# Performance work log

Hardware: AMD Instinct MI355X
Metric: run time of the kernel (lower is better)

Reference implementation:

```python
import jax, jax.numpy as jnp
import numpy as np

SCALES = (0, 1, 2, 3)
SIGMA_NSQ = 2.0
SIGMA_MAX_INV = 4.0 / (255.0 * 255.0)
GAIN_LIMIT = 100.0  # NEG=False
EPS = 1e-10


def gaussian_kernel_2d(N):
    sigma = N / 5.0
    x = jnp.arange(N, dtype=jnp.float32) - (N - 1) / 2.0
    g = jnp.exp(-(x * x) / (2.0 * sigma * sigma))
    k = jnp.outer(g, g)
    return (k / jnp.sum(k))[None, None]  # [1,1,N,N]


def reflect_pad(x, p):
    return jnp.pad(x, ((0, 0), (0, 0), (p, p), (p, p)), mode='reflect')


def conv2d(x, w, stride=1, groups=1):
    return jax.lax.conv_general_dilated(
        x, w, (stride, stride), 'VALID',
        dimension_numbers=('NCHW', 'OIHW', 'NCHW'),
        feature_group_count=groups)


def vif_num_den(ref, dist):
    ref = ref - 128.0
    dist = dist - 128.0
    h, w = ref.shape[-2], ref.shape[-1]
    nums, dens = [], []
    for scale in SCALES:
        N = 2 ** (4 - scale) + 1
        win = gaussian_kernel_2d(N)
        p = (N - 1) // 2
        if scale > 0:
            h, w = h // 2, w // 2
            ref = conv2d(reflect_pad(ref, p), win, stride=2)[:, :, :h, :w]
            dist = conv2d(reflect_pad(dist, p), win, stride=2)[:, :, :h, :w]
        win5 = jnp.tile(win, (5, 1, 1, 1))  # grouped conv, 5 channels
        inp = jnp.concatenate([ref, dist, ref * ref, dist * dist, ref * dist], axis=1)
        out = conv2d(reflect_pad(inp, p), win5, groups=5)  # [b,5,h,w]
        mu1, mu2, s1, s2, s12 = [out[:, i:i + 1] for i in range(5)]
        s1 = jax.nn.relu(s1 - mu1 * mu1)
        s2 = jax.nn.relu(s2 - mu2 * mu2)
        s12 = s12 - mu1 * mu2
        g = s12 / (s1 + EPS)
        sv = s2 - g * s12
        m1 = s1 < EPS
        g = jnp.where(m1, 0.0, g)
        sv = jnp.where(m1, s2, sv)
        s1 = jnp.where(m1, 0.0, s1)
        m2 = s2 < EPS
        g = jnp.where(m2, 0.0, g)
        sv = jnp.where(m2, 0.0, sv)
        sv = jnp.where(g < 0.0, s2, sv)
        g = jax.nn.relu(g)
        sv = jnp.where(sv <= EPS, EPS, sv)
        g = jnp.minimum(g, GAIN_LIMIT)
        num_ar = jnp.log2(1.0 + g * g * s1 / (sv + SIGMA_NSQ))
        den_ar = jnp.log2(1.0 + s1 / SIGMA_NSQ)
        num_ar = jnp.where(s12 < 0.0, 0.0, num_ar)
        m3 = s1 < SIGMA_NSQ
        num_ar = jnp.where(m3, 1.0 - s2 * SIGMA_MAX_INV, num_ar)
        den_ar = jnp.where(m3, 1.0, den_ar)
        nums.append(jnp.sum(num_ar, axis=(-1, -2, -3)))
        dens.append(jnp.sum(den_ar, axis=(-1, -2, -3)))
    return jnp.stack(nums, axis=-1), jnp.stack(dens, axis=-1)


def setup_inputs() -> dict:
    key = jax.random.key(0)
    k1, k2 = jax.random.split(key)
    shape = (4, 1, 1080, 1920)
    ref = jax.random.uniform(k1, shape, dtype=jnp.float32) * 255.0
    dist = jax.random.uniform(k2, shape, dtype=jnp.float32) * 255.0
    return {"ref": ref, "dist": dist}


def reference(ref, dist):
    num, den = vif_num_den(ref, dist)
    return num / den  # VIF features per scale, shape [b, 4]
```

## Files before the change

kernel.cpp:

```cpp
#include <hip/hip_runtime.h>
#include <math.h>

#define VIF_EPS       1e-10f
#define SIGMA_NSQ     2.0f
#define SIGMA_MAX_INV (4.0f / (255.0f * 255.0f))
#define GAIN_LIMIT    100.0f

typedef float v2f __attribute__((ext_vector_type(2)));
typedef float v4f __attribute__((ext_vector_type(4)));

static __device__ __forceinline__ v2f splat2(float s) {
    v2f v; v.x = s; v.y = s; return v;
}

__device__ __forceinline__ int reflect_idx(int i, int n) {
    i = (i < 0) ? -i : i;
    i = (i >= n) ? (2 * n - 2 - i) : i;
    return i;
}

template <int N>
__device__ __forceinline__ void fill_weights_global(float* gw) {
    const float sigma = (float)N / 5.0f;
    const float denom = 2.0f * sigma * sigma;
    float tmp[N];
    float s = 0.0f;
    for (int i = 0; i < N; ++i) {
        float x = (float)i - (float)(N - 1) * 0.5f;
        float g = expf(-(x * x) / denom);
        tmp[i] = g;
        s += g;
    }
    for (int i = 0; i < N; ++i) gw[i] = tmp[i] / s;
}

__global__ __launch_bounds__(64) void init_weights_kernel(float* __restrict__ gw) {
    const int tid = threadIdx.x;
    if (tid == 0) fill_weights_global<17>(gw + 0);
    else if (tid == 1) fill_weights_global<9>(gw + 17);
    else if (tid == 2) fill_weights_global<5>(gw + 26);
    else if (tid == 3) fill_weights_global<3>(gw + 31);
}

__host__ __device__ constexpr int w_off(int N) {
    return (N == 17) ? 0 : (N == 9) ? 17 : (N == 5) ? 26 : 31;
}

constexpr int tile_w(int N) { return (256 - (N - 1)) & ~3; }

template <int N>
struct alignas(16) StatsSmem {
    v2f   a[8][256];
    v2f   bq[8][256];
    float c[8][256];
};
template <int N>
struct alignas(16) DownSmem {
    v2f vb[8][252];
};

template <int N>
__device__ __forceinline__ void stats_body(
    StatsSmem<N>& sm, const float* __restrict__ refp, const float* __restrict__ distp,
    const float* __restrict__ gw,
    int h, int w, float shift, double2* __restrict__ partial,
    int sy, int sx, int bx, int b) {
    constexpr int P   = (N - 1) / 2;
    constexpr int TW  = tile_w(N);
    constexpr int TH  = 8;
    constexpr int LR  = TH + 2 * P;
    constexpr int XG4 = TW / 4;
    constexpr int NT  = TH * XG4;
    constexpr int REPS = (NT + 255) / 256;

    const int tid = threadIdx.x;
    const int ytile = bx % sy;
    const int xtile = bx / sy;
    const int x0 = xtile * TW;
    const int y0 = ytile * TH;

    float wr[N];
#pragma unroll
    for (int j = 0; j < N; ++j) wr[j] = gw[j];

    {
        const int cc = tid;
        const int gx = reflect_idx(x0 + cc - P, w);
        const float* rbase = refp  + (size_t)b * h * w;
        const float* dbase = distp + (size_t)b * h * w;

        float rrow[LR], drow[LR];
        const int rowlo = y0 - P;
        if (rowlo >= 0 && rowlo + LR <= h) {
            unsigned voff = (unsigned)(rowlo * w + gx) * 4u;
            const unsigned vstep = (unsigned)w * 4u;
#pragma unroll
            for (int i = 0; i < LR; ++i) {
                rrow[i] = *(const float*)((const char*)rbase + voff);
                drow[i] = *(const float*)((const char*)dbase + voff);
                voff += vstep;
            }
        } else {
#pragma unroll
            for (int i = 0; i < LR; ++i) {
                const int gy = reflect_idx(rowlo + i, h);
                const size_t o = (size_t)gy * w + gx;
                rrow[i] = rbase[o];
                drow[i] = dbase[o];
            }
        }

        v2f accA[TH], accB[TH];
        float accC[TH];
#pragma unroll
        for (int t = 0; t < TH; ++t) {
            accA[t] = splat2(0.f);
            accB[t] = splat2(0.f);
            accC[t] = 0.f;
        }
#pragma unroll
        for (int i = 0; i < LR; ++i) {
            const float r = rrow[i] - shift;
            const float d = drow[i] - shift;
            v2f rd; rd.x = r; rd.y = d;
            v2f sq = rd * rd;
            const float x = r * d;
#pragma unroll
            for (int t = 0; t < TH; ++t) {
                const int j = i - t;
                if (j >= 0 && j < N) {
                    const float wj = wr[j];
                    accA[t] += splat2(wj) * rd;
                    accB[t] += splat2(wj) * sq;
                    accC[t] += wj * x;
                }
            }
        }
#pragma unroll
        for (int t = 0; t < TH; ++t) {
            sm.a[t][cc]  = accA[t];
            sm.bq[t][cc] = accB[t];
            sm.c[t][cc]  = accC[t];
        }
    }
    __syncthreads();

    float num_v = 0.f, den_v = 0.f;
    {
        constexpr int WC  = N + 3;
        constexpr int F4C = (WC + 3) / 4;
#pragma unroll
        for (int rep = 0; rep < REPS; ++rep) {
            const int task = tid + 256 * rep;
            if (task < NT) {
                const int row = task / XG4;
                const int xg  = task - row * XG4;

                v2f muA[4], muB[4];
                float muC[4];
#pragma unroll
                for (int q = 0; q < 4; ++q) {
                    muA[q] = splat2(0.f);
                    muB[q] = splat2(0.f);
                    muC[q] = 0.f;
                }

                const v4f* A4 = (const v4f*)&sm.a[row][xg * 4];
                const v4f* B4 = (const v4f*)&sm.bq[row][xg * 4];
#pragma unroll
                for (int f = 0; f < WC / 2; ++f) {
                    v4f ta = A4[f];
                    v4f tb = B4[f];
#pragma unroll
                    for (int hlf = 0; hlf < 2; ++hlf) {
                        const int k = 2 * f + hlf;
                        v2f pa = hlf ? __builtin_shufflevector(ta, ta, 2, 3)
                                     : __builtin_shufflevector(ta, ta, 0, 1);
                        v2f pb = hlf ? __builtin_shufflevector(tb, tb, 2, 3)
                                     : __builtin_shufflevector(tb, tb, 0, 1);
#pragma unroll
                        for (int q = 0; q < 4; ++q) {
                            const int j = k - q;
                            if (j >= 0 && j < N) {
                                const float wj = wr[j];
                                muA[q] += splat2(wj) * pa;
                                muB[q] += splat2(wj) * pb;
                            }
                        }
                    }
                }
                {
                    const v4f* C4 = (const v4f*)&sm.c[row][xg * 4];
#pragma unroll
                    for (int f = 0; f < F4C; ++f) {
                        v4f t = C4[f];
#pragma unroll
                        for (int e = 0; e < 4; ++e) {
                            const int k = 4 * f + e;
                            const float x = (e == 0) ? t.x : (e == 1) ? t.y
                                          : (e == 2) ? t.z : t.w;
#pragma unroll
                            for (int q = 0; q < 4; ++q) {
                                const int j = k - q;
                                if (j >= 0 && j < N) muC[q] += wr[j] * x;
                            }
                        }
                    }
                }

                const int gy = y0 + row;
#pragma unroll
                for (int q = 0; q < 4; ++q) {
                    int gx = x0 + xg * 4 + q;
                    if (gx < w && gy < h) {
                        float mu1 = muA[q].x, mu2 = muA[q].y;
                        float s1  = fmaxf(0.f, muB[q].x - mu1 * mu1);
                        float s2  = fmaxf(0.f, muB[q].y - mu2 * mu2);
                        float s12 = muC[q] - mu1 * mu2;

                        float g  = s12 / (s1 + VIF_EPS);
                        float sv = s2 - g * s12;
                        if (s1 < VIF_EPS) { g = 0.f; sv = s2; s1 = 0.f; }
                        if (s2 < VIF_EPS) { g = 0.f; sv = 0.f; }
                        if (g  < 0.f)     { sv = s2; g = 0.f; }
                        if (sv <= VIF_EPS) sv = VIF_EPS;
                        g = fminf(g, GAIN_LIMIT);

                        float num_ar = __log2f(1.f + g * g * s1 / (sv + SIGMA_NSQ));
                        float den_ar = __log2f(1.f + s1 / SIGMA_NSQ);
                        if (s12 < 0.f) num_ar = 0.f;
                        if (s1 < SIGMA_NSQ) { num_ar = 1.f - s2 * SIGMA_MAX_INV; den_ar = 1.f; }
                        num_v += num_ar;
                        den_v += den_ar;
                    }
                }
            }
        }
    }

#pragma unroll
    for (int off = 32; off > 0; off >>= 1) {
        num_v += __shfl_down(num_v, off);
        den_v += __shfl_down(den_v, off);
    }
    __syncthreads();
    float* rs = reinterpret_cast<float*>(&sm);
    const int wid = tid >> 6, lane = tid & 63;
    if (lane == 0) { rs[wid] = num_v; rs[4 + wid] = den_v; }
    __syncthreads();
    if (tid == 0) {
        float ns = rs[0] + rs[1] + rs[2] + rs[3];
        float ds = rs[4] + rs[5] + rs[6] + rs[7];
        partial[(size_t)b * (sy * sx) + bx] = make_double2((double)ns, (double)ds);
    }
}

template <int N>
__device__ __forceinline__ void down_body(
    DownSmem<N>& sm, const float* __restrict__ rin, const float* __restrict__ din,
    const float* __restrict__ gw,
    float* __restrict__ rout, float* __restrict__ dout,
    int h, int w, int h2, int w2, float shift, int dgx, int bx, int b) {
    constexpr int P   = (N - 1) / 2;
    constexpr int TOW = 120, TOH = 8;
    constexpr int IC  = 2 * (TOW - 1) + N;
    constexpr int NR  = 2 * (TOH - 1) + N;
    constexpr int XG4 = TOW / 4;
    constexpr int WL  = N + 6;

    float wr[N];
#pragma unroll
    for (int j = 0; j < N; ++j) wr[j] = gw[j];

    const int tid = threadIdx.x;
    const int xt  = bx % dgx;
    const int yt  = bx / dgx;
    const int x0  = xt * TOW;
    const int y0  = yt * TOH;

    if (tid < IC) {
        const int gx = reflect_idx(2 * x0 - P + tid, w);
        const int rowlo = 2 * y0 - P;
        const float* rbase = rin + (size_t)b * h * w;
        const float* dbase = din + (size_t)b * h * w;

        float rr[NR], dd[NR];
        const bool interior = (rowlo >= 0) && (rowlo + NR <= h);
        if (interior) {
            unsigned voff = (unsigned)(rowlo * w + gx) * 4u;
            const unsigned vstep = (unsigned)w * 4u;
#pragma unroll
            for (int i = 0; i < NR; ++i) {
                rr[i] = *(const float*)((const char*)rbase + voff);
                dd[i] = *(const float*)((const char*)dbase + voff);
                voff += vstep;
            }
        } else {
#pragma unroll
            for (int i = 0; i < NR; ++i) {
                const int gy = reflect_idx(rowlo + i, h);
                const size_t o = (size_t)gy * w + gx;
                rr[i] = rbase[o];
                dd[i] = dbase[o];
            }
        }

        v2f acc[TOH];
#pragma unroll
        for (int t = 0; t < TOH; ++t) acc[t] = splat2(0.f);
#pragma unroll
        for (int i = 0; i < NR; ++i) {
            v2f x; x.x = rr[i] - shift; x.y = dd[i] - shift;
#pragma unroll
            for (int t = 0; t < TOH; ++t) {
                const int j = i - 2 * t;
                if (j >= 0 && j < N) acc[t] += splat2(wr[j]) * x;
            }
        }
#pragma unroll
        for (int t = 0; t < TOH; ++t) sm.vb[t][tid] = acc[t];
    }
    __syncthreads();

    if (tid < TOH * XG4) {
        const int row = tid / XG4;
        const int xg  = tid - row * XG4;

        v2f o[4];
#pragma unroll
        for (int q = 0; q < 4; ++q) o[q] = splat2(0.f);

        const v4f* s4 = (const v4f*)&sm.vb[row][8 * xg];
#pragma unroll
        for (int f = 0; f < (WL + 1) / 2; ++f) {
            v4f t = s4[f];
#pragma unroll
            for (int hlf = 0; hlf < 2; ++hlf) {
                const int k = 2 * f + hlf;
                v2f p = hlf ? __builtin_shufflevector(t, t, 2, 3)
                            : __builtin_shufflevector(t, t, 0, 1);
#pragma unroll
                for (int q = 0; q < 4; ++q) {
                    const int j = k - 2 * q;
                    if (j >= 0 && j < N) o[q] += splat2(wr[j]) * p;
                }
            }
        }
        const int gy = y0 + row;
        if (gy < h2) {
            float* rp = rout + (size_t)b * h2 * w2 + (size_t)gy * w2 + x0 + 4 * xg;
            float* dp = dout + (size_t)b * h2 * w2 + (size_t)gy * w2 + x0 + 4 * xg;
            *(float4*)rp = make_float4(o[0].x, o[1].x, o[2].x, o[3].x);
            *(float4*)dp = make_float4(o[0].y, o[1].y, o[2].y, o[3].y);
        }
    }
}

template <int NS, int ND>
__global__ __launch_bounds__(256) void fused_kernel(
    const float* __restrict__ sref, const float* __restrict__ sdist,
    const float* __restrict__ gw,
    int sh, int sw, float sshift, double2* __restrict__ partial, int sy, int sx,
    float* __restrict__ drout, float* __restrict__ ddout,
    int dh2, int dw2, int dgx, int nStats) {
    __shared__ union {
        StatsSmem<NS> s;
        DownSmem<ND>  d;
    } u;
    const int bx = blockIdx.x;
    const int b  = blockIdx.z;
    if (bx < nStats)
        stats_body<NS>(u.s, sref, sdist, gw + w_off(NS), sh, sw, sshift,
                       partial, sy, sx, bx, b);
    else
        down_body<ND>(u.d, sref, sdist, gw + w_off(ND), drout, ddout,
                      sh, sw, dh2, dw2, sshift, dgx, bx - nStats, b);
}

template <int N>
__global__ __launch_bounds__(256) void stats_only_kernel(
    const float* __restrict__ refp, const float* __restrict__ distp,
    const float* __restrict__ gw,
    int h, int w, float shift, double2* __restrict__ partial, int sy, int sx) {
    __shared__ StatsSmem<N> sm;
    stats_body<N>(sm, refp, distp, gw + w_off(N), h, w, shift, partial,
                  sy, sx, blockIdx.x, blockIdx.z);
}

__global__ __launch_bounds__(256) void reduce_kernel(
    const double2* __restrict__ part, float* __restrict__ out,
    int4 bases, int4 counts) {
    __shared__ double sn[4], sd[4];
    const int s = blockIdx.x & 3;
    const int b = blockIdx.x >> 2;
    const int base = (&bases.x)[s];
    const int cnt  = (&counts.x)[s];
    const double2* p = part + base + (size_t)b * cnt;

    double ns = 0.0, ds = 0.0;
    for (int i = threadIdx.x; i < cnt; i += 256) {
        double2 v = p[i];
        ns += v.x;
        ds += v.y;
    }
#pragma unroll
    for (int off = 32; off > 0; off >>= 1) {
        ns += __shfl_down(ns, off);
        ds += __shfl_down(ds, off);
    }
    const int wid = threadIdx.x >> 6, lane = threadIdx.x & 63;
    if (lane == 0) { sn[wid] = ns; sd[wid] = ds; }
    __syncthreads();
    if (threadIdx.x == 0) {
        double Nv = sn[0] + sn[1] + sn[2] + sn[3];
        double Dv = sd[0] + sd[1] + sd[2] + sd[3];
        out[b * 4 + s] = (float)(Nv / Dv);
    }
}

extern "C" void kernel_launch(void* const* d_in, const int* in_sizes, int n_in,
                              void* d_out, int out_size, void* d_ws, size_t ws_size,
                              hipStream_t stream) {
    const float* ref  = (const float*)d_in[0];
    const float* dist = (const float*)d_in[1];
    float* out = (float*)d_out;

    const int B = 4;
    const int H0 = 1080, W0 = 1920;
    const int H1 = 540,  W1 = 960;
    const int H2 = 270,  W2 = 480;
    const int H3 = 135,  W3 = 240;

    char*  ws  = (char*)d_ws;
    size_t off = 0;
    auto alloc = [&](size_t bytes) -> void* {
        void* p = ws + off;
        off += (bytes + 255) & ~(size_t)255;
        return p;
    };
    float* gw    = (float*)alloc(34 * sizeof(float));
    float* ref1  = (float*)alloc((size_t)B * H1 * W1 * 4);
    float* dist1 = (float*)alloc((size_t)B * H1 * W1 * 4);
    float* ref2  = (float*)alloc((size_t)B * H2 * W2 * 4);
    float* dist2 = (float*)alloc((size_t)B * H2 * W2 * 4);
    float* ref3  = (float*)alloc((size_t)B * H3 * W3 * 4);
    float* dist3 = (float*)alloc((size_t)B * H3 * W3 * 4);

    const int sx0 = (W0 + tile_w(17) - 1) / tile_w(17), sy0 = (H0 + 7) / 8;
    const int sx1 = (W1 + tile_w(9)  - 1) / tile_w(9),  sy1 = (H1 + 7) / 8;
    const int sx2 = (W2 + tile_w(5)  - 1) / tile_w(5),  sy2 = (H2 + 7) / 8;
    const int sx3 = (W3 + tile_w(3)  - 1) / tile_w(3),  sy3 = (H3 + 7) / 8;
    const int n0 = sx0 * sy0, n1 = sx1 * sy1, n2 = sx2 * sy2, n3 = sx3 * sy3;

    const int dgx1 = W1 / 120, nD1 = dgx1 * ((H1 + 7) / 8);
    const int dgx2 = W2 / 120, nD2 = dgx2 * ((H2 + 7) / 8);
    const int dgx3 = W3 / 120, nD3 = dgx3 * ((H3 + 7) / 8);

    double2* part = (double2*)alloc((size_t)B * (n0 + n1 + n2 + n3) * sizeof(double2));
    double2* p0 = part;
    double2* p1 = p0 + (size_t)B * n0;
    double2* p2 = p1 + (size_t)B * n1;
    double2* p3 = p2 + (size_t)B * n2;

    dim3 blk(256);

    init_weights_kernel<<<1, 64, 0, stream>>>(gw);

    fused_kernel<17, 9><<<dim3(n0 + nD1, 1, B), blk, 0, stream>>>(
        ref, dist, gw, H0, W0, 128.0f, p0, sy0, sx0,
        ref1, dist1, H1, W1, dgx1, n0);

    fused_kernel<9, 5><<<dim3(n1 + nD2, 1, B), blk, 0, stream>>>(
        ref1, dist1, gw, H1, W1, 0.0f, p1, sy1, sx1,
        ref2, dist2, H2, W2, dgx2, n1);

    fused_kernel<5, 3><<<dim3(n2 + nD3, 1, B), blk, 0, stream>>>(
        ref2, dist2, gw, H2, W2, 0.0f, p2, sy2, sx2,
        ref3, dist3, H3, W3, dgx3, n2);

    stats_only_kernel<3><<<dim3(n3, 1, B), blk, 0, stream>>>(
        ref3, dist3, gw, H3, W3, 0.0f, p3, sy3, sx3);

    reduce_kernel<<<16, 256, 0, stream>>>(
        part, out,
        make_int4(0, B * n0, B * (n0 + n1), B * (n0 + n1 + n2)),
        make_int4(n0, n1, n2, n3));
}
```

Before: 171.3 us.

## Shrink stats shared-memory staging to five rows with a two-phase reuse

The stats kernel now stores only five rows of vertical-pass results in shared memory instead of eight. It first computes the horizontal pass for rows 0-4, then overwrites slots 0-2 with rows 5-7 (row 4 stays in slot 4) and handles the remaining tasks. The smaller shared-memory footprint is meant to let more blocks fit per CU. In exchange it adds an extra barrier, and keeps the row 5-7 accumulators live in registers across the first phase, which may raise register pressure.

```diff
diff --git a/kernel.cpp b/kernel.cpp
--- a/kernel.cpp
+++ b/kernel.cpp
@@ -50,9 +50,9 @@
 
 template <int N>
 struct alignas(16) StatsSmem {
-    v2f   a[8][256];
-    v2f   bq[8][256];
-    float c[8][256];
+    v2f   a[5][256];
+    v2f   bq[5][256];
+    float c[5][256];
 };
 template <int N>
 struct alignas(16) DownSmem {
@@ -71,7 +71,7 @@
     constexpr int LR  = TH + 2 * P;
     constexpr int XG4 = TW / 4;
     constexpr int NT  = TH * XG4;
-    constexpr int REPS = (NT + 255) / 256;
+    static_assert(5 * XG4 >= 256, "phase 2a tasks must fit rows 0..4");
 
     const int tid = threadIdx.x;
     const int ytile = bx % sy;
@@ -83,6 +83,8 @@
 #pragma unroll
     for (int j = 0; j < N; ++j) wr[j] = gw[j];
 
+    v2f accA[TH], accB[TH];
+    float accC[TH];
     {
         const int cc = tid;
         const int gx = reflect_idx(x0 + cc - P, w);
@@ -110,8 +112,6 @@
             }
         }
 
-        v2f accA[TH], accB[TH];
-        float accC[TH];
 #pragma unroll
         for (int t = 0; t < TH; ++t) {
             accA[t] = splat2(0.f);
@@ -137,104 +137,121 @@
             }
         }
 #pragma unroll
-        for (int t = 0; t < TH; ++t) {
-            sm.a[t][cc]  = accA[t];
-            sm.bq[t][cc] = accB[t];
-            sm.c[t][cc]  = accC[t];
+        for (int t = 0; t < 5; ++t) {
+            sm.a[t][tid]  = accA[t];
+            sm.bq[t][tid] = accB[t];
+            sm.c[t][tid]  = accC[t];
         }
     }
     __syncthreads();
 
     float num_v = 0.f, den_v = 0.f;
-    {
-        constexpr int WC  = N + 3;
-        constexpr int F4C = (WC + 3) / 4;
-#pragma unroll
-        for (int rep = 0; rep < REPS; ++rep) {
-            const int task = tid + 256 * rep;
-            if (task < NT) {
-                const int row = task / XG4;
-                const int xg  = task - row * XG4;
-
-                v2f muA[4], muB[4];
-                float muC[4];
+    constexpr int WC  = N + 3;
+    constexpr int F4C = (WC + 3) / 4;
+
+    auto do_task = [&](int task, int slot) {
+        const int row = task / XG4;
+        const int xg  = task - row * XG4;
+
+        v2f muA[4], muB[4];
+        float muC[4];
+#pragma unroll
+        for (int q = 0; q < 4; ++q) {
+            muA[q] = splat2(0.f);
+            muB[q] = splat2(0.f);
+            muC[q] = 0.f;
+        }
+
+        const v4f* A4 = (const v4f*)&sm.a[slot][xg * 4];
+        const v4f* B4 = (const v4f*)&sm.bq[slot][xg * 4];
+#pragma unroll
+        for (int f = 0; f < WC / 2; ++f) {
+            v4f ta = A4[f];
+            v4f tb = B4[f];
+#pragma unroll
+            for (int hlf = 0; hlf < 2; ++hlf) {
+                const int k = 2 * f + hlf;
+                v2f pa = hlf ? __builtin_shufflevector(ta, ta, 2, 3)
+                             : __builtin_shufflevector(ta, ta, 0, 1);
+                v2f pb = hlf ? __builtin_shufflevector(tb, tb, 2, 3)
+                             : __builtin_shufflevector(tb, tb, 0, 1);
 #pragma unroll
                 for (int q = 0; q < 4; ++q) {
-                    muA[q] = splat2(0.f);
-                    muB[q] = splat2(0.f);
-                    muC[q] = 0.f;
-                }
-
-                const v4f* A4 = (const v4f*)&sm.a[row][xg * 4];
-                const v4f* B4 = (const v4f*)&sm.bq[row][xg * 4];
-#pragma unroll
-                for (int f = 0; f < WC / 2; ++f) {
-                    v4f ta = A4[f];
-                    v4f tb = B4[f];
-#pragma unroll
-                    for (int hlf = 0; hlf < 2; ++hlf) {
-                        const int k = 2 * f + hlf;
-                        v2f pa = hlf ? __builtin_shufflevector(ta, ta, 2, 3)
-                                     : __builtin_shufflevector(ta, ta, 0, 1);
-                        v2f pb = hlf ? __builtin_shufflevector(tb, tb, 2, 3)
-                                     : __builtin_shufflevector(tb, tb, 0, 1);
-#pragma unroll
-                        for (int q = 0; q < 4; ++q) {
-                            const int j = k - q;
-                            if (j >= 0 && j < N) {
-                                const float wj = wr[j];
-                                muA[q] += splat2(wj) * pa;
-                                muB[q] += splat2(wj) * pb;
-                            }
-                        }
+                    const int j = k - q;
+                    if (j >= 0 && j < N) {
+                        const float wj = wr[j];
+                        muA[q] += splat2(wj) * pa;
+                        muB[q] += splat2(wj) * pb;
                     }
                 }
-                {
-                    const v4f* C4 = (const v4f*)&sm.c[row][xg * 4];
-#pragma unroll
-                    for (int f = 0; f < F4C; ++f) {
-                        v4f t = C4[f];
-#pragma unroll
-                        for (int e = 0; e < 4; ++e) {
-                            const int k = 4 * f + e;
-                            const float x = (e == 0) ? t.x : (e == 1) ? t.y
-                                          : (e == 2) ? t.z : t.w;
-#pragma unroll
-                            for (int q = 0; q < 4; ++q) {
-                                const int j = k - q;
-                                if (j >= 0 && j < N) muC[q] += wr[j] * x;
-                            }
-                        }
+            }
+        }
+        {
+            const v4f* C4 = (const v4f*)&sm.c[slot][xg * 4];
+#pragma unroll
+            for (int f = 0; f < F4C; ++f) {
+                v4f t = C4[f];
+#pragma unroll
+                for (int e = 0; e < 4; ++e) {
+                    const int k = 4 * f + e;
+                    const float x = (e == 0) ? t.x : (e == 1) ? t.y
+                                  : (e == 2) ? t.z : t.w;
+#pragma unroll
+                    for (int q = 0; q < 4; ++q) {
+                        const int j = k - q;
+                        if (j >= 0 && j < N) muC[q] += wr[j] * x;
                     }
                 }
-
-                const int gy = y0 + row;
-#pragma unroll
-                for (int q = 0; q < 4; ++q) {
-                    int gx = x0 + xg * 4 + q;
-                    if (gx < w && gy < h) {
-                        float mu1 = muA[q].x, mu2 = muA[q].y;
-                        float s1  = fmaxf(0.f, muB[q].x - mu1 * mu1);
-                        float s2  = fmaxf(0.f, muB[q].y - mu2 * mu2);
-                        float s12 = muC[q] - mu1 * mu2;
-
-                        float g  = s12 / (s1 + VIF_EPS);
-                        float sv = s2 - g * s12;
-                        if (s1 < VIF_EPS) { g = 0.f; sv = s2; s1 = 0.f; }
-                        if (s2 < VIF_EPS) { g = 0.f; sv = 0.f; }
-                        if (g  < 0.f)     { sv = s2; g = 0.f; }
-                        if (sv <= VIF_EPS) sv = VIF_EPS;
-                        g = fminf(g, GAIN_LIMIT);
-
-                        float num_ar = __log2f(1.f + g * g * s1 / (sv + SIGMA_NSQ));
-                        float den_ar = __log2f(1.f + s1 / SIGMA_NSQ);
-                        if (s12 < 0.f) num_ar = 0.f;
-                        if (s1 < SIGMA_NSQ) { num_ar = 1.f - s2 * SIGMA_MAX_INV; den_ar = 1.f; }
-                        num_v += num_ar;
-                        den_v += den_ar;
-                    }
-                }
-            }
+            }
+        }
+
+        const int gy = y0 + row;
+#pragma unroll
+        for (int q = 0; q < 4; ++q) {
+            int gx = x0 + xg * 4 + q;
+            if (gx < w && gy < h) {
+                float mu1 = muA[q].x, mu2 = muA[q].y;
+                float s1  = fmaxf(0.f, muB[q].x - mu1 * mu1);
+                float s2  = fmaxf(0.f, muB[q].y - mu2 * mu2);
+                float s12 = muC[q] - mu1 * mu2;
+
+                float g  = s12 / (s1 + VIF_EPS);
+                float sv = s2 - g * s12;
+                if (s1 < VIF_EPS) { g = 0.f; sv = s2; s1 = 0.f; }
+                if (s2 < VIF_EPS) { g = 0.f; sv = 0.f; }
+                if (g  < 0.f)     { sv = s2; g = 0.f; }
+                if (sv <= VIF_EPS) sv = VIF_EPS;
+                g = fminf(g, GAIN_LIMIT);
+
+                float num_ar = __log2f(1.f + g * g * s1 / (sv + SIGMA_NSQ));
+                float den_ar = __log2f(1.f + s1 / SIGMA_NSQ);
+                if (s12 < 0.f) num_ar = 0.f;
+                if (s1 < SIGMA_NSQ) { num_ar = 1.f - s2 * SIGMA_MAX_INV; den_ar = 1.f; }
+                num_v += num_ar;
+                den_v += den_ar;
+            }
+        }
+    };
+
+    {
+        const int task = tid;
+        do_task(task, task / XG4);
+    }
+    __syncthreads();
+
+#pragma unroll
+    for (int t = 5; t < TH; ++t) {
+        sm.a[t - 5][tid]  = accA[t];
+        sm.bq[t - 5][tid] = accB[t];
+        sm.c[t - 5][tid]  = accC[t];
+    }
+    __syncthreads();
+
+    {
+        const int task = tid + 256;
+        if (task < NT) {
+            const int row = task / XG4;
+            do_task(task, (row == 4) ? 4 : (row - 5));
         }
     }
 
```

New measurement: 184.7 us. 1.08x slower.
